# Kernel optimization log

Hardware: AMD Instinct MI355X
Metric: run time of the kernel (lower is better)

Reference implementation:

```python
import jax, jax.numpy as jnp
import numpy as np

N = 100000      # nodes
E = 3200000     # edges
F_IN = 256      # in_channels
H = 64          # hidden_channels
C = 2           # out_channels
G = 128         # graphs in batch


def setup_inputs() -> dict:
    key = jax.random.key(0)
    ks = jax.random.split(key, 10)
    x = jax.random.normal(ks[0], (N, F_IN), jnp.float32)
    edge_index = jax.random.randint(ks[1], (2, E), 0, N, dtype=jnp.int64)
    batch = jnp.sort(jax.random.randint(ks[2], (N,), 0, G, dtype=jnp.int64))
    s = 0.05
    W1 = jax.random.normal(ks[3], (F_IN, H), jnp.float32) * s
    b1 = jnp.zeros((H,), jnp.float32)
    W2 = jax.random.normal(ks[4], (H, H), jnp.float32) * s
    b2 = jnp.zeros((H,), jnp.float32)
    fc_W = jax.random.normal(ks[5], (H, C), jnp.float32) * s
    fc_b = jnp.zeros((C,), jnp.float32)
    return {"x": x, "edge_index": edge_index, "batch": batch,
            "W1": W1, "b1": b1, "W2": W2, "b2": b2,
            "fc_W": fc_W, "fc_b": fc_b}


def _gcn_layer(h, src, dst, norm, W, b, n_nodes):
    # PyG GCNConv: linear transform first, then normalized aggregate, then bias
    h = h @ W                                   # [N, H]
    msg = h[src] * norm[:, None]                # [E+N, H] gather + scale
    out = jax.ops.segment_sum(msg, dst, num_segments=n_nodes)
    return out + b


def reference(x, edge_index, batch, W1, b1, W2, b2, fc_W, fc_b):
    n_nodes = x.shape[0]
    # add self loops (GCNConv default)
    loop = jnp.arange(n_nodes, dtype=edge_index.dtype)
    src = jnp.concatenate([edge_index[0], loop])
    dst = jnp.concatenate([edge_index[1], loop])
    # symmetric normalization D^{-1/2} (A+I) D^{-1/2}
    deg = jax.ops.segment_sum(jnp.ones_like(src, dtype=x.dtype), dst,
                              num_segments=n_nodes)
    deg_isqrt = jnp.where(deg > 0, jax.lax.rsqrt(deg), 0.0)
    norm = deg_isqrt[src] * deg_isqrt[dst]

    h = jax.nn.relu(_gcn_layer(x, src, dst, norm, W1, b1, n_nodes))
    h = jax.nn.relu(_gcn_layer(h, src, dst, norm, W2, b2, n_nodes))

    # global mean pool over graphs
    n_graphs = G
    sums = jax.ops.segment_sum(h, batch, num_segments=n_graphs)
    cnts = jax.ops.segment_sum(jnp.ones((n_nodes,), h.dtype), batch,
                               num_segments=n_graphs)
    pooled = sums / jnp.clip(cnts, 1.0)[:, None]  # [G, H]
    return pooled @ fc_W + fc_b                   # [G, C]
```

## Files before the change

kernel.cpp:

```cpp
#include <hip/hip_runtime.h>
#include <hip/hip_bf16.h>


#define F_IN 256
#define HDIM 64
#define BR_SHIFT 7
#define BRANGE 128
#define BCAP 4608
#define CHUNK 8192
#define NBK 788
#define HS_SCALE 32.0f

typedef short short8 __attribute__((ext_vector_type(8)));
typedef short short4v __attribute__((ext_vector_type(4)));
typedef float float4v __attribute__((ext_vector_type(4)));

__device__ __forceinline__ unsigned bf16_rn(float f) {
  unsigned u = __builtin_bit_cast(unsigned, f);
  return (u + 0x7FFFu + ((u >> 16) & 1u)) >> 16;
}
__device__ __forceinline__ float bf16_to_f32(unsigned h) {
  return __builtin_bit_cast(float, h << 16);
}
__device__ __forceinline__ unsigned char f32_to_fp8(float v) {
  unsigned r = (unsigned)__builtin_amdgcn_cvt_pk_fp8_f32(v, v, 0, false);
  return (unsigned char)(r & 0xFF);
}
__device__ __forceinline__ float4v fp8x4_to_f32x4(unsigned u) {
  float4v r;
  r[0] = __builtin_amdgcn_cvt_f32_fp8(u, 0);
  r[1] = __builtin_amdgcn_cvt_f32_fp8(u, 1);
  r[2] = __builtin_amdgcn_cvt_f32_fp8(u, 2);
  r[3] = __builtin_amdgcn_cvt_f32_fp8(u, 3);
  return r;
}

__global__ __launch_bounds__(256) void bin_kernel(
    const int* __restrict__ src, const int* __restrict__ dst,
    int* __restrict__ gcur, int* __restrict__ entries, int E, int nb) {
  __shared__ int out32[CHUNK];
  __shared__ int pref[NBK + 1];
  __shared__ int cur[NBK];
  __shared__ int gbase[NBK];
  __shared__ int sscan[256];
  const int tid = threadIdx.x;
  for (int i = tid; i < nb; i += 256) cur[i] = 0;
  __syncthreads();
  long e0 = (long)blockIdx.x * CHUNK;
  int cnt = (int)min((long)CHUNK, (long)E - e0);
  for (int i = tid; i < cnt; i += 256)
    atomicAdd(&cur[dst[e0 + i] >> BR_SHIFT], 1);
  __syncthreads();
  int b0 = tid * 4;
  int h[4];
  int s = 0;
#pragma unroll
  for (int i = 0; i < 4; ++i) {
    h[i] = (b0 + i < nb) ? cur[b0 + i] : 0;
    s += h[i];
  }
  int x = s;
  sscan[tid] = x;
  __syncthreads();
  for (int off = 1; off < 256; off <<= 1) {
    int t = (tid >= off) ? sscan[tid - off] : 0;
    __syncthreads();
    sscan[tid] += t;
    __syncthreads();
  }
  int run = sscan[tid] - x;
#pragma unroll
  for (int i = 0; i < 4; ++i) {
    if (b0 + i < nb) {
      pref[b0 + i] = run;
      cur[b0 + i] = run;
      if (h[i] > 0) gbase[b0 + i] = atomicAdd(&gcur[b0 + i], h[i]);
      run += h[i];
    }
  }
  if (tid == 0) pref[nb] = cnt;
  __syncthreads();
  for (int i = tid; i < cnt; i += 256) {
    int d = dst[e0 + i];
    int sv = src[e0 + i];
    int b = d >> BR_SHIFT;
    int r = atomicAdd(&cur[b], 1);
    out32[r] = ((d & (BRANGE - 1)) << 17) | sv;
  }
  __syncthreads();
  for (int j = tid; j < cnt; j += 256) {
    int lo = 0, hi = nb - 1;
    while (lo < hi) {
      int mid = (lo + hi + 1) >> 1;
      if (pref[mid] <= j) lo = mid; else hi = mid - 1;
    }
    int b = lo;
    int slot = gbase[b] + (j - pref[b]);
    if (slot < BCAP) entries[(size_t)b * BCAP + slot] = out32[j];
  }
}

__global__ __launch_bounds__(256) void bucket_scan_kernel(
    const int* __restrict__ gcur, int* __restrict__ bbase,
    int* __restrict__ rowptr, int nb, int N, int E) {
  __shared__ int sscan[256];
  const int tid = threadIdx.x;
  int b0 = tid * 4;
  int h[4];
  int s = 0;
#pragma unroll
  for (int i = 0; i < 4; ++i) {
    h[i] = (b0 + i < nb) ? min(gcur[b0 + i], BCAP) : 0;
    s += h[i];
  }
  int x = s;
  sscan[tid] = x;
  __syncthreads();
  for (int off = 1; off < 256; off <<= 1) {
    int t = (tid >= off) ? sscan[tid - off] : 0;
    __syncthreads();
    sscan[tid] += t;
    __syncthreads();
  }
  int run = sscan[tid] - x;
#pragma unroll
  for (int i = 0; i < 4; ++i) {
    if (b0 + i < nb) {
      bbase[b0 + i] = run;
      run += h[i];
    }
  }
  if (tid == 0) rowptr[N] = E;
}

__global__ __launch_bounds__(256) void csr_build_kernel(
    const int* __restrict__ entries, const int* __restrict__ gcur,
    const int* __restrict__ bbase, int* __restrict__ rowptr,
    float* __restrict__ dnorm, int* __restrict__ csr, int N) {
  __shared__ int lbuf[BCAP];
  __shared__ int lcnt[BRANGE];
  __shared__ int lpref[BRANGE];
  __shared__ int lcur[BRANGE];
  const int b = blockIdx.x, tid = threadIdx.x;
  const int v0 = b * BRANGE;
  const int nloc = min(BRANGE, N - v0);
  if (tid < BRANGE) lcnt[tid] = 0;
  __syncthreads();
  const int cnt = min(gcur[b], BCAP);
  const int base = bbase[b];
  const int* ep = entries + (size_t)b * BCAP;
  for (int i = tid; i < cnt; i += 256) atomicAdd(&lcnt[ep[i] >> 17], 1);
  __syncthreads();
  if (tid < BRANGE) lpref[tid] = lcnt[tid];
  __syncthreads();
  for (int off = 1; off < BRANGE; off <<= 1) {
    int t = 0;
    if (tid < BRANGE && tid >= off) t = lpref[tid - off];
    __syncthreads();
    if (tid < BRANGE) lpref[tid] += t;
    __syncthreads();
  }
  if (tid < BRANGE) {
    int excl = lpref[tid] - lcnt[tid];
    lcur[tid] = excl;
    if (tid < nloc) {
      rowptr[v0 + tid] = base + excl;
      dnorm[v0 + tid] = rsqrtf((float)lcnt[tid] + 1.0f);
    }
  }
  __syncthreads();
  for (int i = tid; i < cnt; i += 256) {
    int e = ep[i];
    int dl = e >> 17;
    int pos = atomicAdd(&lcur[dl], 1);
    if (pos < BCAP) lbuf[pos] = e & 0x1FFFF;
  }
  __syncthreads();
  int* outp = csr + base;
  for (int i = tid; i < cnt; i += 256) outp[i] = lbuf[i];
}

template <int K>
__global__ __launch_bounds__(256) void wfrag_kernel(
    const float* __restrict__ W, short* __restrict__ whi,
    short* __restrict__ wlo) {
  constexpr int KS = K / 32;
  int slot = blockIdx.x * 256 + threadIdx.x;
  if (slot >= 4 * KS * 64 * 8) return;
  int j = slot & 7;
  int lane = (slot >> 3) & 63;
  int fk = slot >> 9;
  int ks = fk % KS;
  int ct = fk / KS;
  int k = ks * 32 + (lane >> 4) * 8 + j;
  int n = ct * 16 + (lane & 15);
  float w = W[k * 64 + n];
  unsigned h = bf16_rn(w);
  unsigned l = bf16_rn(w - bf16_to_f32(h));
  whi[slot] = (short)h;
  wlo[slot] = (short)l;
}

template <int K>
__global__ __launch_bounds__(512) void mfma_gemm_kernel(
    const float* __restrict__ X, const short* __restrict__ whi,
    const short* __restrict__ wlo, const float* __restrict__ dnorm,
    unsigned char* __restrict__ out, int N) {
  constexpr int KS = K / 32;
  constexpr int P = K + 8;
  __shared__ __align__(16) short Ahi[64 * P];
  __shared__ __align__(16) short Alo[64 * P];
  const int tid = threadIdx.x;
  const long base = (long)blockIdx.x * 64;
  constexpr int C4 = K / 4;
  constexpr int NL = 64 * C4 / 512;
#pragma unroll
  for (int i = 0; i < NL; ++i) {
    int idx = tid + i * 512;
    int row = idx / C4;
    int c4 = idx % C4;
    long r = base + row;
    if (r >= N) r = N - 1;
    float4v v = *(const float4v*)&X[(size_t)r * K + c4 * 4];
    short4v hv, lv;
#pragma unroll
    for (int j = 0; j < 4; ++j) {
      float f = v[j];
      unsigned h = bf16_rn(f);
      unsigned l = bf16_rn(f - bf16_to_f32(h));
      hv[j] = (short)h;
      lv[j] = (short)l;
    }
    *(short4v*)&Ahi[row * P + c4 * 4] = hv;
    *(short4v*)&Alo[row * P + c4 * 4] = lv;
  }
  __syncthreads();
  const int lane = tid & 63;
  const int wave = tid >> 6;
  const int rt = wave & 3;
  const int chalf = wave >> 2;
  const int m = lane & 15;
  const int q = lane >> 4;
  const int arow = rt * 16 + m;
  float4v acc[2];
  acc[0] = (float4v){0.f, 0.f, 0.f, 0.f};
  acc[1] = (float4v){0.f, 0.f, 0.f, 0.f};
  for (int ks = 0; ks < KS; ++ks) {
    int koff = ks * 32 + q * 8;
    short8 ah = *(const short8*)&Ahi[arow * P + koff];
    short8 al = *(const short8*)&Alo[arow * P + koff];
#pragma unroll
    for (int cc = 0; cc < 2; ++cc) {
      int ct = chalf * 2 + cc;
      size_t fo = ((size_t)(ct * KS + ks) * 64 + lane) * 8;
      short8 bh = *(const short8*)&whi[fo];
      short8 bl = *(const short8*)&wlo[fo];
      acc[cc] = __builtin_amdgcn_mfma_f32_16x16x32_bf16(ah, bh, acc[cc], 0, 0, 0);
      acc[cc] = __builtin_amdgcn_mfma_f32_16x16x32_bf16(ah, bl, acc[cc], 0, 0, 0);
      acc[cc] = __builtin_amdgcn_mfma_f32_16x16x32_bf16(al, bh, acc[cc], 0, 0, 0);
    }
  }
#pragma unroll
  for (int reg = 0; reg < 4; ++reg) {
    long grow = base + rt * 16 + q * 4 + reg;
    if (grow < N) {
      float dn = dnorm[grow] * HS_SCALE;
#pragma unroll
      for (int cc = 0; cc < 2; ++cc) {
        int ct = chalf * 2 + cc;
        out[grow * 64 + ct * 16 + m] = f32_to_fp8(acc[cc][reg] * dn);
      }
    }
  }
}

struct VolReg {
  unsigned u0, u1, u2, u3, u4, u5, u6, u7;
  float s0, s1, s2, s3, s4, s5, s6, s7;
};

__device__ __forceinline__ VolReg volley_issue(
    const unsigned char* __restrict__ hs, const int* __restrict__ csr,
    int j, int end, int v, int g, size_t co) {
  VolReg r;
  const int rr = end - j;
#define GCN_ISSUE(u, U, S)                                                 \
  {                                                                        \
    int t0 = csr[j + 4 * (u)], t1 = csr[j + 4 * (u) + 1],                  \
        t2 = csr[j + 4 * (u) + 2], t3 = csr[j + 4 * (u) + 3];              \
    int idx = g == 0 ? t0 : (g == 1 ? t1 : (g == 2 ? t2 : t3));            \
    bool p = (4 * (u) + g) < rr;                                           \
    idx = p ? idx : v;                                                     \
    S = p ? 1.0f : 0.0f;                                                   \
    U = *(const unsigned*)(hs + (((size_t)idx) << 6) + co);                \
  }
  GCN_ISSUE(0, r.u0, r.s0)
  GCN_ISSUE(1, r.u1, r.s1)
  GCN_ISSUE(2, r.u2, r.s2)
  GCN_ISSUE(3, r.u3, r.s3)
  GCN_ISSUE(4, r.u4, r.s4)
  GCN_ISSUE(5, r.u5, r.s5)
  GCN_ISSUE(6, r.u6, r.s6)
  GCN_ISSUE(7, r.u7, r.s7)
#undef GCN_ISSUE
  return r;
}

__device__ __forceinline__ void volley_acc(const VolReg& r, float4v& a0,
                                           float4v& a1, float4v& a2,
                                           float4v& a3) {
  a0 += fp8x4_to_f32x4(r.u0) * r.s0;
  a1 += fp8x4_to_f32x4(r.u1) * r.s1;
  a2 += fp8x4_to_f32x4(r.u2) * r.s2;
  a3 += fp8x4_to_f32x4(r.u3) * r.s3;
  a0 += fp8x4_to_f32x4(r.u4) * r.s4;
  a1 += fp8x4_to_f32x4(r.u5) * r.s5;
  a2 += fp8x4_to_f32x4(r.u6) * r.s6;
  a3 += fp8x4_to_f32x4(r.u7) * r.s7;
}

__device__ __forceinline__ float4v fold4(float4v a0, float4v a1, float4v a2,
                                         float4v a3) {
  float4v t = (a0 + a1) + (a2 + a3);
#pragma unroll
  for (int k = 0; k < 4; ++k) {
    float x = t[k];
    x += __shfl_xor(x, 16);
    x += __shfl_xor(x, 32);
    t[k] = x;
  }
  return t;
}

__device__ __forceinline__ float4v node_out(
    const unsigned char* __restrict__ hs, const float* __restrict__ dnorm,
    const float* __restrict__ bias, float4v t, int v, int q) {
  unsigned su = *(const unsigned*)(hs + (((size_t)v) << 6) + (q << 2));
  float4v sf = fp8x4_to_f32x4(su);
  float dn = dnorm[v] * (1.0f / HS_SCALE);
  float4v b4 = *(const float4v*)&bias[q << 2];
  float4v o;
#pragma unroll
  for (int k = 0; k < 4; ++k) o[k] = fmaxf(dn * (t[k] + sf[k]) + b4[k], 0.f);
  return o;
}

__global__ __launch_bounds__(256) void gather_agg_kernel(
    const unsigned char* __restrict__ hs, const int* __restrict__ rowptr,
    const int* __restrict__ csr, const float* __restrict__ dnorm,
    const float* __restrict__ bias, float* __restrict__ hout, int N) {
  const int lane = threadIdx.x & 63;
  const int wave = __builtin_amdgcn_readfirstlane((int)(threadIdx.x >> 6));
  const int g = lane >> 4;
  const int q = lane & 15;
  const size_t co = (size_t)(q << 2);
  int v0 = blockIdx.x * 8 + wave * 2;
  if (v0 >= N) return;
  int v1 = v0 + 1;
  bool hasB = v1 < N;
  int beg0 = rowptr[v0];
  int end0 = rowptr[v0 + 1];
  int beg1 = end0;
  int end1 = hasB ? rowptr[v1 + 1] : end0;

  float4v z = {0.f, 0.f, 0.f, 0.f};
  float4v aA0 = z, aA1 = z, aA2 = z, aA3 = z;
  float4v aB0 = z, aB1 = z, aB2 = z, aB3 = z;

  VolReg rA = volley_issue(hs, csr, beg0, end0, v0, g, co);
  VolReg rB;
  if (hasB) rB = volley_issue(hs, csr, beg1, end1, v1, g, co);
  volley_acc(rA, aA0, aA1, aA2, aA3);
  if (hasB) volley_acc(rB, aB0, aB1, aB2, aB3);

  bool tA = beg0 + 32 < end0;
  bool tB = hasB && (beg1 + 32 < end1);
  if (tA || tB) {
    VolReg r2A, r2B;
    if (tA) r2A = volley_issue(hs, csr, beg0 + 32, end0, v0, g, co);
    if (tB) r2B = volley_issue(hs, csr, beg1 + 32, end1, v1, g, co);
    if (tA) volley_acc(r2A, aA0, aA1, aA2, aA3);
    if (tB) volley_acc(r2B, aB0, aB1, aB2, aB3);
  }
  for (int j = beg0 + 64; j < end0; j += 32) {
    VolReg r = volley_issue(hs, csr, j, end0, v0, g, co);
    volley_acc(r, aA0, aA1, aA2, aA3);
  }
  if (hasB)
    for (int j = beg1 + 64; j < end1; j += 32) {
      VolReg r = volley_issue(hs, csr, j, end1, v1, g, co);
      volley_acc(r, aB0, aB1, aB2, aB3);
    }

  float4v oA = node_out(hs, dnorm, bias, fold4(aA0, aA1, aA2, aA3), v0, q);
  if (g == 0) *(float4v*)&hout[((size_t)v0 << 6) + (q << 2)] = oA;
  if (hasB) {
    float4v oB = node_out(hs, dnorm, bias, fold4(aB0, aB1, aB2, aB3), v1, q);
    if (g == 0) *(float4v*)&hout[((size_t)v1 << 6) + (q << 2)] = oB;
  }
}

__global__ __launch_bounds__(256) void gather_agg_pool_kernel(
    const unsigned char* __restrict__ hs, const int* __restrict__ rowptr,
    const int* __restrict__ csr, const float* __restrict__ dnorm,
    const float* __restrict__ bias, const int* __restrict__ batch,
    float* __restrict__ pooled, int N) {
  const int lane = threadIdx.x & 63;
  const int wave = __builtin_amdgcn_readfirstlane((int)(threadIdx.x >> 6));
  const int g = lane >> 4;
  const int q = lane & 15;
  const size_t co = (size_t)(q << 2);
  int v0 = blockIdx.x * 8 + wave * 2;
  if (v0 >= N) return;
  int v1 = v0 + 1;
  bool hasB = v1 < N;
  int beg0 = rowptr[v0];
  int end0 = rowptr[v0 + 1];
  int beg1 = end0;
  int end1 = hasB ? rowptr[v1 + 1] : end0;

  float4v z = {0.f, 0.f, 0.f, 0.f};
  float4v aA0 = z, aA1 = z, aA2 = z, aA3 = z;
  float4v aB0 = z, aB1 = z, aB2 = z, aB3 = z;

  VolReg rA = volley_issue(hs, csr, beg0, end0, v0, g, co);
  VolReg rB;
  if (hasB) rB = volley_issue(hs, csr, beg1, end1, v1, g, co);
  volley_acc(rA, aA0, aA1, aA2, aA3);
  if (hasB) volley_acc(rB, aB0, aB1, aB2, aB3);

  bool tA = beg0 + 32 < end0;
  bool tB = hasB && (beg1 + 32 < end1);
  if (tA || tB) {
    VolReg r2A, r2B;
    if (tA) r2A = volley_issue(hs, csr, beg0 + 32, end0, v0, g, co);
    if (tB) r2B = volley_issue(hs, csr, beg1 + 32, end1, v1, g, co);
    if (tA) volley_acc(r2A, aA0, aA1, aA2, aA3);
    if (tB) volley_acc(r2B, aB0, aB1, aB2, aB3);
  }
  for (int j = beg0 + 64; j < end0; j += 32) {
    VolReg r = volley_issue(hs, csr, j, end0, v0, g, co);
    volley_acc(r, aA0, aA1, aA2, aA3);
  }
  if (hasB)
    for (int j = beg1 + 64; j < end1; j += 32) {
      VolReg r = volley_issue(hs, csr, j, end1, v1, g, co);
      volley_acc(r, aB0, aB1, aB2, aB3);
    }

  {
    float4v o = node_out(hs, dnorm, bias, fold4(aA0, aA1, aA2, aA3), v0, q);
    int srcl = lane >> 2;
    float w0 = __shfl(o[0], srcl);
    float w1 = __shfl(o[1], srcl);
    float w2 = __shfl(o[2], srcl);
    float w3 = __shfl(o[3], srcl);
    int k = lane & 3;
    float val = k == 0 ? w0 : (k == 1 ? w1 : (k == 2 ? w2 : w3));
    int b = batch[v0];
    atomicAdd(&pooled[((size_t)b << 6) + lane], val);
  }
  if (hasB) {
    float4v o = node_out(hs, dnorm, bias, fold4(aB0, aB1, aB2, aB3), v1, q);
    int srcl = lane >> 2;
    float w0 = __shfl(o[0], srcl);
    float w1 = __shfl(o[1], srcl);
    float w2 = __shfl(o[2], srcl);
    float w3 = __shfl(o[3], srcl);
    int k = lane & 3;
    float val = k == 0 ? w0 : (k == 1 ? w1 : (k == 2 ? w2 : w3));
    int b = batch[v1];
    atomicAdd(&pooled[((size_t)b << 6) + lane], val);
  }
}

__global__ __launch_bounds__(256) void final_fc_kernel(
    const float* __restrict__ pooled, const int* __restrict__ batch,
    const float* __restrict__ fcW, const float* __restrict__ fcb,
    float* __restrict__ out, int G, int N) {
  int t = blockIdx.x * 256 + threadIdx.x;
  if (t < G * 2) {
    int g = t >> 1, c = t & 1;
    int lo = 0, hi = N;
    while (lo < hi) { int m = (lo + hi) >> 1; if (batch[m] < g) lo = m + 1; else hi = m; }
    int lb = lo;
    lo = 0; hi = N;
    while (lo < hi) { int m = (lo + hi) >> 1; if (batch[m] <= g) lo = m + 1; else hi = m; }
    int cntg = lo - lb;
    float inv = 1.0f / fmaxf((float)cntg, 1.0f);
    float acc = fcb[c];
#pragma unroll
    for (int h = 0; h < 64; ++h)
      acc = fmaf(pooled[g * 64 + h] * inv, fcW[h * 2 + c], acc);
    out[t] = acc;
  }
}

extern "C" void kernel_launch(void* const* d_in, const int* in_sizes, int n_in,
                              void* d_out, int out_size, void* d_ws, size_t ws_size,
                              hipStream_t stream) {
  const float* x   = (const float*)d_in[0];
  const int*   ei  = (const int*)d_in[1];
  const int*   bat = (const int*)d_in[2];
  const float* W1  = (const float*)d_in[3];
  const float* b1  = (const float*)d_in[4];
  const float* W2  = (const float*)d_in[5];
  const float* b2  = (const float*)d_in[6];
  const float* fcW = (const float*)d_in[7];
  const float* fcb = (const float*)d_in[8];
  float* out = (float*)d_out;

  const int N = in_sizes[0] / F_IN;
  const int E = in_sizes[1] / 2;
  const int G = out_size / 2;
  const int* src = ei;
  const int* dst = ei + E;
  const int nb  = (N + BRANGE - 1) >> BR_SHIFT;

  auto aln = [](size_t v) { return (v + 63) & ~(size_t)63; };
  char* w = (char*)d_ws;
  int*    entries = (int*)w;     w += aln((size_t)nb * BCAP * 4);
  int*    gcur    = (int*)w;     w += aln((size_t)nb * 4);
  int*    bbase   = (int*)w;     w += aln((size_t)nb * 4);
  int*    rowptr  = (int*)w;     w += aln((size_t)(N + 1) * 4);
  float*  dnorm   = (float*)w;   w += aln((size_t)N * 4);
  int*    csr     = (int*)w;     w += aln((size_t)(E + 64) * 4);
  unsigned char* hs = (unsigned char*)w; w += aln((size_t)N * 64);
  float*  h1      = (float*)w;   w += aln((size_t)N * 64 * 4);
  float*  pooled  = (float*)w;   w += aln((size_t)G * 64 * 4);
  short*  whi1    = (short*)w;   w += aln((size_t)F_IN * 64 * 2);
  short*  wlo1    = (short*)w;   w += aln((size_t)F_IN * 64 * 2);
  short*  whi2    = (short*)w;   w += aln((size_t)HDIM * 64 * 2);
  short*  wlo2    = (short*)w;   w += aln((size_t)HDIM * 64 * 2);

  hipMemsetAsync(gcur, 0, (size_t)nb * 4, stream);
  hipMemsetAsync(pooled, 0, (size_t)G * 64 * 4, stream);

  wfrag_kernel<F_IN><<<(F_IN * 64 * 8 / 8 + 255) / 256, 256, 0, stream>>>(W1, whi1, wlo1);
  wfrag_kernel<HDIM><<<(HDIM * 64 * 8 / 8 + 255) / 256, 256, 0, stream>>>(W2, whi2, wlo2);

  bin_kernel<<<(E + CHUNK - 1) / CHUNK, 256, 0, stream>>>(
      src, dst, gcur, entries, E, nb);
  bucket_scan_kernel<<<1, 256, 0, stream>>>(gcur, bbase, rowptr, nb, N, E);
  csr_build_kernel<<<nb, 256, 0, stream>>>(entries, gcur, bbase, rowptr,
                                           dnorm, csr, N);

  mfma_gemm_kernel<F_IN><<<(N + 63) / 64, 512, 0, stream>>>(
      x, whi1, wlo1, dnorm, hs, N);
  gather_agg_kernel<<<(N + 7) / 8, 256, 0, stream>>>(hs, rowptr, csr, dnorm, b1, h1, N);

  mfma_gemm_kernel<HDIM><<<(N + 63) / 64, 512, 0, stream>>>(
      h1, whi2, wlo2, dnorm, hs, N);
  gather_agg_pool_kernel<<<(N + 7) / 8, 256, 0, stream>>>(hs, rowptr, csr, dnorm, b2, bat, pooled, N);

  final_fc_kernel<<<1, 256, 0, stream>>>(pooled, bat, fcW, fcb, out, G, N);
}
```

Before: 504.4 us.

## Gather 64 neighbors per round with a zero-row sentinel instead of masked scaling

The gather loops now issue 16 loads per lane per round, covering 64 edges instead of 32. Out-of-range slots point to a zeroed sentinel row appended after the last node, which removes the per-element 0/1 scale multiply. Both nodes' first rounds are issued up front, but the rest of node B's tail work now runs only after node A finishes. The aim is more memory-level parallelism and fewer ALU ops per edge, at the cost of higher register pressure and wasted loads for nodes with fewer than 64 edges. Average degree is about 33, so most rounds are roughly half padding.

```diff
diff --git a/kernel.cpp b/kernel.cpp
--- a/kernel.cpp
+++ b/kernel.cpp
@@ -274,49 +274,34 @@
   }
 }
 
-struct VolReg {
-  unsigned u0, u1, u2, u3, u4, u5, u6, u7;
-  float s0, s1, s2, s3, s4, s5, s6, s7;
+struct Round {
+  unsigned u[16];
 };
 
-__device__ __forceinline__ VolReg volley_issue(
+__device__ __forceinline__ Round issue_round(
     const unsigned char* __restrict__ hs, const int* __restrict__ csr,
-    int j, int end, int v, int g, size_t co) {
-  VolReg r;
-  const int rr = end - j;
-#define GCN_ISSUE(u, U, S)                                                 \
-  {                                                                        \
-    int t0 = csr[j + 4 * (u)], t1 = csr[j + 4 * (u) + 1],                  \
-        t2 = csr[j + 4 * (u) + 2], t3 = csr[j + 4 * (u) + 3];              \
-    int idx = g == 0 ? t0 : (g == 1 ? t1 : (g == 2 ? t2 : t3));            \
-    bool p = (4 * (u) + g) < rr;                                           \
-    idx = p ? idx : v;                                                     \
-    S = p ? 1.0f : 0.0f;                                                   \
-    U = *(const unsigned*)(hs + (((size_t)idx) << 6) + co);                \
-  }
-  GCN_ISSUE(0, r.u0, r.s0)
-  GCN_ISSUE(1, r.u1, r.s1)
-  GCN_ISSUE(2, r.u2, r.s2)
-  GCN_ISSUE(3, r.u3, r.s3)
-  GCN_ISSUE(4, r.u4, r.s4)
-  GCN_ISSUE(5, r.u5, r.s5)
-  GCN_ISSUE(6, r.u6, r.s6)
-  GCN_ISSUE(7, r.u7, r.s7)
-#undef GCN_ISSUE
+    int beg, int deg, int zrow, int g, size_t co) {
+  Round r;
+#pragma unroll
+  for (int u = 0; u < 16; ++u) {
+    int slot = 4 * u + g;
+    int raw = csr[beg + slot];
+    int idx = slot < deg ? raw : zrow;
+    r.u[u] = *(const unsigned*)(hs + (((size_t)idx) << 6) + co);
+  }
   return r;
 }
 
-__device__ __forceinline__ void volley_acc(const VolReg& r, float4v& a0,
-                                           float4v& a1, float4v& a2,
-                                           float4v& a3) {
-  a0 += fp8x4_to_f32x4(r.u0) * r.s0;
-  a1 += fp8x4_to_f32x4(r.u1) * r.s1;
-  a2 += fp8x4_to_f32x4(r.u2) * r.s2;
-  a3 += fp8x4_to_f32x4(r.u3) * r.s3;
-  a0 += fp8x4_to_f32x4(r.u4) * r.s4;
-  a1 += fp8x4_to_f32x4(r.u5) * r.s5;
-  a2 += fp8x4_to_f32x4(r.u6) * r.s6;
-  a3 += fp8x4_to_f32x4(r.u7) * r.s7;
+__device__ __forceinline__ void decode_round(const Round& r, float4v& a0,
+                                             float4v& a1, float4v& a2,
+                                             float4v& a3) {
+#pragma unroll
+  for (int u = 0; u < 16; u += 4) {
+    a0 += fp8x4_to_f32x4(r.u[u + 0]);
+    a1 += fp8x4_to_f32x4(r.u[u + 1]);
+    a2 += fp8x4_to_f32x4(r.u[u + 2]);
+    a3 += fp8x4_to_f32x4(r.u[u + 3]);
+  }
 }
 
 __device__ __forceinline__ float4v fold4(float4v a0, float4v a1, float4v a2,
@@ -354,7 +339,7 @@
   const int g = lane >> 4;
   const int q = lane & 15;
   const size_t co = (size_t)(q << 2);
-  int v0 = blockIdx.x * 8 + wave * 2;
+  int v0 = (blockIdx.x * 4 + wave) * 2;
   if (v0 >= N) return;
   int v1 = v0 + 1;
   bool hasB = v1 < N;
@@ -362,40 +347,30 @@
   int end0 = rowptr[v0 + 1];
   int beg1 = end0;
   int end1 = hasB ? rowptr[v1 + 1] : end0;
+  int d0 = end0 - beg0, d1 = end1 - beg1;
+
+  Round rA = issue_round(hs, csr, beg0, d0, N, g, co);
+  Round rB;
+  if (hasB) rB = issue_round(hs, csr, beg1, d1, N, g, co);
 
   float4v z = {0.f, 0.f, 0.f, 0.f};
-  float4v aA0 = z, aA1 = z, aA2 = z, aA3 = z;
-  float4v aB0 = z, aB1 = z, aB2 = z, aB3 = z;
-
-  VolReg rA = volley_issue(hs, csr, beg0, end0, v0, g, co);
-  VolReg rB;
-  if (hasB) rB = volley_issue(hs, csr, beg1, end1, v1, g, co);
-  volley_acc(rA, aA0, aA1, aA2, aA3);
-  if (hasB) volley_acc(rB, aB0, aB1, aB2, aB3);
-
-  bool tA = beg0 + 32 < end0;
-  bool tB = hasB && (beg1 + 32 < end1);
-  if (tA || tB) {
-    VolReg r2A, r2B;
-    if (tA) r2A = volley_issue(hs, csr, beg0 + 32, end0, v0, g, co);
-    if (tB) r2B = volley_issue(hs, csr, beg1 + 32, end1, v1, g, co);
-    if (tA) volley_acc(r2A, aA0, aA1, aA2, aA3);
-    if (tB) volley_acc(r2B, aB0, aB1, aB2, aB3);
-  }
-  for (int j = beg0 + 64; j < end0; j += 32) {
-    VolReg r = volley_issue(hs, csr, j, end0, v0, g, co);
-    volley_acc(r, aA0, aA1, aA2, aA3);
-  }
-  if (hasB)
-    for (int j = beg1 + 64; j < end1; j += 32) {
-      VolReg r = volley_issue(hs, csr, j, end1, v1, g, co);
-      volley_acc(r, aB0, aB1, aB2, aB3);
-    }
-
-  float4v oA = node_out(hs, dnorm, bias, fold4(aA0, aA1, aA2, aA3), v0, q);
+  float4v a0 = z, a1 = z, a2 = z, a3 = z;
+  decode_round(rA, a0, a1, a2, a3);
+  for (int j = 64; j < d0; j += 64) {
+    Round rt = issue_round(hs, csr, beg0 + j, d0 - j, N, g, co);
+    decode_round(rt, a0, a1, a2, a3);
+  }
+  float4v oA = node_out(hs, dnorm, bias, fold4(a0, a1, a2, a3), v0, q);
   if (g == 0) *(float4v*)&hout[((size_t)v0 << 6) + (q << 2)] = oA;
+
   if (hasB) {
-    float4v oB = node_out(hs, dnorm, bias, fold4(aB0, aB1, aB2, aB3), v1, q);
+    float4v b0 = z, b1 = z, b2 = z, b3 = z;
+    decode_round(rB, b0, b1, b2, b3);
+    for (int j = 64; j < d1; j += 64) {
+      Round rt = issue_round(hs, csr, beg1 + j, d1 - j, N, g, co);
+      decode_round(rt, b0, b1, b2, b3);
+    }
+    float4v oB = node_out(hs, dnorm, bias, fold4(b0, b1, b2, b3), v1, q);
     if (g == 0) *(float4v*)&hout[((size_t)v1 << 6) + (q << 2)] = oB;
   }
 }
@@ -410,7 +385,7 @@
   const int g = lane >> 4;
   const int q = lane & 15;
   const size_t co = (size_t)(q << 2);
-  int v0 = blockIdx.x * 8 + wave * 2;
+  int v0 = (blockIdx.x * 4 + wave) * 2;
   if (v0 >= N) return;
   int v1 = v0 + 1;
   bool hasB = v1 < N;
@@ -418,38 +393,21 @@
   int end0 = rowptr[v0 + 1];
   int beg1 = end0;
   int end1 = hasB ? rowptr[v1 + 1] : end0;
+  int d0 = end0 - beg0, d1 = end1 - beg1;
+
+  Round rA = issue_round(hs, csr, beg0, d0, N, g, co);
+  Round rB;
+  if (hasB) rB = issue_round(hs, csr, beg1, d1, N, g, co);
 
   float4v z = {0.f, 0.f, 0.f, 0.f};
-  float4v aA0 = z, aA1 = z, aA2 = z, aA3 = z;
-  float4v aB0 = z, aB1 = z, aB2 = z, aB3 = z;
-
-  VolReg rA = volley_issue(hs, csr, beg0, end0, v0, g, co);
-  VolReg rB;
-  if (hasB) rB = volley_issue(hs, csr, beg1, end1, v1, g, co);
-  volley_acc(rA, aA0, aA1, aA2, aA3);
-  if (hasB) volley_acc(rB, aB0, aB1, aB2, aB3);
-
-  bool tA = beg0 + 32 < end0;
-  bool tB = hasB && (beg1 + 32 < end1);
-  if (tA || tB) {
-    VolReg r2A, r2B;
-    if (tA) r2A = volley_issue(hs, csr, beg0 + 32, end0, v0, g, co);
-    if (tB) r2B = volley_issue(hs, csr, beg1 + 32, end1, v1, g, co);
-    if (tA) volley_acc(r2A, aA0, aA1, aA2, aA3);
-    if (tB) volley_acc(r2B, aB0, aB1, aB2, aB3);
-  }
-  for (int j = beg0 + 64; j < end0; j += 32) {
-    VolReg r = volley_issue(hs, csr, j, end0, v0, g, co);
-    volley_acc(r, aA0, aA1, aA2, aA3);
-  }
-  if (hasB)
-    for (int j = beg1 + 64; j < end1; j += 32) {
-      VolReg r = volley_issue(hs, csr, j, end1, v1, g, co);
-      volley_acc(r, aB0, aB1, aB2, aB3);
-    }
-
+  float4v a0 = z, a1 = z, a2 = z, a3 = z;
+  decode_round(rA, a0, a1, a2, a3);
+  for (int j = 64; j < d0; j += 64) {
+    Round rt = issue_round(hs, csr, beg0 + j, d0 - j, N, g, co);
+    decode_round(rt, a0, a1, a2, a3);
+  }
   {
-    float4v o = node_out(hs, dnorm, bias, fold4(aA0, aA1, aA2, aA3), v0, q);
+    float4v o = node_out(hs, dnorm, bias, fold4(a0, a1, a2, a3), v0, q);
     int srcl = lane >> 2;
     float w0 = __shfl(o[0], srcl);
     float w1 = __shfl(o[1], srcl);
@@ -461,7 +419,13 @@
     atomicAdd(&pooled[((size_t)b << 6) + lane], val);
   }
   if (hasB) {
-    float4v o = node_out(hs, dnorm, bias, fold4(aB0, aB1, aB2, aB3), v1, q);
+    float4v b0 = z, b1 = z, b2 = z, b3 = z;
+    decode_round(rB, b0, b1, b2, b3);
+    for (int j = 64; j < d1; j += 64) {
+      Round rt = issue_round(hs, csr, beg1 + j, d1 - j, N, g, co);
+      decode_round(rt, b0, b1, b2, b3);
+    }
+    float4v o = node_out(hs, dnorm, bias, fold4(b0, b1, b2, b3), v1, q);
     int srcl = lane >> 2;
     float w0 = __shfl(o[0], srcl);
     float w1 = __shfl(o[1], srcl);
@@ -525,7 +489,7 @@
   int*    rowptr  = (int*)w;     w += aln((size_t)(N + 1) * 4);
   float*  dnorm   = (float*)w;   w += aln((size_t)N * 4);
   int*    csr     = (int*)w;     w += aln((size_t)(E + 64) * 4);
-  unsigned char* hs = (unsigned char*)w; w += aln((size_t)N * 64);
+  unsigned char* hs = (unsigned char*)w; w += aln((size_t)(N + 1) * 64);
   float*  h1      = (float*)w;   w += aln((size_t)N * 64 * 4);
   float*  pooled  = (float*)w;   w += aln((size_t)G * 64 * 4);
   short*  whi1    = (short*)w;   w += aln((size_t)F_IN * 64 * 2);
@@ -535,6 +499,7 @@
 
   hipMemsetAsync(gcur, 0, (size_t)nb * 4, stream);
   hipMemsetAsync(pooled, 0, (size_t)G * 64 * 4, stream);
+  hipMemsetAsync(hs + (size_t)N * 64, 0, 64, stream);
 
   wfrag_kernel<F_IN><<<(F_IN * 64 * 8 / 8 + 255) / 256, 256, 0, stream>>>(W1, whi1, wlo1);
   wfrag_kernel<HDIM><<<(HDIM * 64 * 8 / 8 + 255) / 256, 256, 0, stream>>>(W2, whi2, wlo2);
```

New measurement: 485.8 us. -3.7%, faster.
